# Kernel optimization log

Hardware: AMD Instinct MI355X
Metric: run time of the kernel (lower is better)

## Reference

```python
import jax, jax.numpy as jnp
import numpy as np

DIM = 768
HEADS = 12
HEAD_DIM = DIM // HEADS
HIDDEN = 4 * DIM
SCALE = HEAD_DIM ** -0.5
LN_EPS = 1e-5


def _fit_poly_gelu():
    # replicate PolyGELU.__init__: quadratic least-squares fit to exact GELU on [-3,3]
    x = np.linspace(-3.0, 3.0, 10000).astype(np.float32)
    y = np.asarray(jax.nn.gelu(jnp.asarray(x), approximate=False))
    X = np.stack([x ** 2, x, np.ones_like(x)], axis=1)
    c, *_ = np.linalg.lstsq(X, y, rcond=None)
    return c.astype(np.float32)  # [a, b, c]


def setup_inputs() -> dict:
    key = jax.random.key(0)
    ks = jax.random.split(key, 8)
    g = _fit_poly_gelu()
    w = lambda k, shp: (jax.random.normal(k, shp, dtype=jnp.float32) * 0.02)
    return {
        "x": jax.random.normal(ks[0], (4, 2048, DIM), dtype=jnp.float32),
        "ln1_g": jnp.ones((DIM,), jnp.float32),
        "ln1_b": jnp.zeros((DIM,), jnp.float32),
        "ln2_g": jnp.ones((DIM,), jnp.float32),
        "ln2_b": jnp.zeros((DIM,), jnp.float32),
        "qkv_w": w(ks[1], (DIM, 3 * DIM)),   # stored [in, out]
        "qkv_b": jnp.zeros((3 * DIM,), jnp.float32),
        "proj_w": w(ks[2], (DIM, DIM)),
        "proj_b": jnp.zeros((DIM,), jnp.float32),
        "fc1_w": w(ks[3], (DIM, HIDDEN)),
        "fc1_b": jnp.zeros((HIDDEN,), jnp.float32),
        "fc2_w": w(ks[4], (HIDDEN, DIM)),
        "fc2_b": jnp.zeros((DIM,), jnp.float32),
        "attn_a": jnp.float32(0.05),
        "attn_b": jnp.float32(0.5),
        "attn_c": jnp.float32(0.25),
        "gelu_a": jnp.float32(g[0]),
        "gelu_b": jnp.float32(g[1]),
        "gelu_c": jnp.float32(g[2]),
    }


def _layernorm(x, gamma, beta):
    mu = jnp.mean(x, axis=-1, keepdims=True)
    var = jnp.mean(jnp.square(x - mu), axis=-1, keepdims=True)
    return (x - mu) / jnp.sqrt(var + LN_EPS) * gamma + beta


def reference(x, ln1_g, ln1_b, ln2_g, ln2_b, qkv_w, qkv_b, proj_w, proj_b,
              fc1_w, fc1_b, fc2_w, fc2_b, attn_a, attn_b, attn_c,
              gelu_a, gelu_b, gelu_c):
    B, N, C = x.shape
    # --- attention branch ---
    h = _layernorm(x, ln1_g, ln1_b)
    qkv = (h @ qkv_w + qkv_b).reshape(B, N, 3, HEADS, HEAD_DIM)
    q, k, v = (qkv[:, :, i].transpose(0, 2, 1, 3) for i in range(3))  # [B,H,N,D]
    attn = jnp.einsum("bhnd,bhmd->bhnm", q, k) * SCALE
    # poly_normed: quadratic activation, clamp, row-normalize
    attn = attn_a * attn * attn + attn_b * attn + attn_c
    attn = jnp.maximum(attn, 1e-6)
    attn = attn / (jnp.sum(attn, axis=-1, keepdims=True) + 1e-8)
    out = jnp.einsum("bhnm,bhmd->bhnd", attn, v).transpose(0, 2, 1, 3).reshape(B, N, C)
    x = x + (out @ proj_w + proj_b)
    # --- MLP branch with PolyGELU ---
    h = _layernorm(x, ln2_g, ln2_b)
    u = h @ fc1_w + fc1_b
    u = gelu_a * u * u + gelu_b * u + gelu_c
    x = x + (u @ fc2_w + fc2_b)
    return x
```

## Files before the change

### kernel.cpp

```cpp
#include <hip/hip_runtime.h>

typedef __bf16 bf16x8 __attribute__((ext_vector_type(8)));
typedef __bf16 bf16x4 __attribute__((ext_vector_type(4)));
typedef float f32x4 __attribute__((ext_vector_type(4)));

#define LN_EPS 1e-5f

__device__ __forceinline__ void gl2lds16(const void* g, void* l) {
  __builtin_amdgcn_global_load_lds(
      (const __attribute__((address_space(1))) unsigned int*)g,
      (__attribute__((address_space(3))) unsigned int*)l, 16, 0, 0);
}

__global__ __launch_bounds__(256) void transpose_k(const float* __restrict__ in,
                                                   __bf16* __restrict__ out,
                                                   int R, int C) {
  __shared__ __bf16 t[32][33];
  int tx = threadIdx.x & 31, ty = threadIdx.x >> 5;
  int c = blockIdx.x * 32 + tx;
  for (int j = 0; j < 4; j++) {
    int r = blockIdx.y * 32 + ty + j * 8;
    t[ty + j * 8][tx] = (__bf16)in[(size_t)r * C + c];
  }
  __syncthreads();
  int r2 = blockIdx.y * 32 + tx;
  for (int j = 0; j < 4; j++) {
    int c2 = blockIdx.x * 32 + ty + j * 8;
    out[(size_t)c2 * R + r2] = t[tx][ty + j * 8];
  }
}

__global__ __launch_bounds__(256) void transpose_v(const __bf16* __restrict__ qkv,
                                                   __bf16* __restrict__ vt) {
  __shared__ __bf16 t[32][33];
  int bh = blockIdx.z;
  int b = bh / 12, h = bh % 12;
  int n0 = blockIdx.x * 32, d0 = blockIdx.y * 32;
  int tx = threadIdx.x & 31, ty = threadIdx.x >> 5;
  for (int j = 0; j < 4; j++) {
    int n = n0 + ty + j * 8;
    t[ty + j * 8][tx] = qkv[(size_t)(b * 2048 + n) * 2304 + 1536 + h * 64 + d0 + tx];
  }
  __syncthreads();
  for (int j = 0; j < 4; j++) {
    int d = d0 + ty + j * 8;
    vt[((size_t)bh * 64 + d) * 2048 + n0 + tx] = t[tx][ty + j * 8];
  }
}

__global__ __launch_bounds__(256) void ln_kernel(const float* __restrict__ x,
                                                 const float* __restrict__ g,
                                                 const float* __restrict__ bta,
                                                 __bf16* __restrict__ out) {
  int row = blockIdx.x;
  size_t base = (size_t)row * 768;
  int t = threadIdx.x;
  float v[3];
  float s = 0.f, s2 = 0.f;
  for (int k = 0; k < 3; k++) {
    float f = x[base + t + k * 256];
    v[k] = f;
    s += f;
    s2 += f * f;
  }
  for (int m = 1; m < 64; m <<= 1) {
    s += __shfl_xor(s, m, 64);
    s2 += __shfl_xor(s2, m, 64);
  }
  __shared__ float sm[4][2];
  int wid = t >> 6, lane = t & 63;
  if (lane == 0) { sm[wid][0] = s; sm[wid][1] = s2; }
  __syncthreads();
  s = sm[0][0] + sm[1][0] + sm[2][0] + sm[3][0];
  s2 = sm[0][1] + sm[1][1] + sm[2][1] + sm[3][1];
  float mu = s * (1.f / 768.f);
  float var = s2 * (1.f / 768.f) - mu * mu;
  float rstd = rsqrtf(var + LN_EPS);
  for (int k = 0; k < 3; k++) {
    int c = t + k * 256;
    out[base + c] = (__bf16)((v[k] - mu) * rstd * g[c] + bta[c]);
  }
}

template <int EPI>
__global__ __launch_bounds__(256) void gemm128(const __bf16* __restrict__ A,
                                               const __bf16* __restrict__ BT,
                                               const float* __restrict__ bias,
                                               const float* __restrict__ res,
                                               void* __restrict__ outv,
                                               int M, int N, int K,
                                               const float* __restrict__ c0p,
                                               const float* __restrict__ c1p,
                                               const float* __restrict__ c2p) {
  __shared__ __bf16 As[128][32];
  __shared__ __bf16 Bs[128][32];
  int tid = threadIdx.x;
  int lane = tid & 63, wid = tid >> 6;
  int wr = wid >> 1, wc = wid & 1;
  int m0 = blockIdx.y * 128, n0 = blockIdx.x * 128;
  int mr = lane & 15, kq = (lane >> 4) * 8;
  int srow = tid >> 2, scol = (tid & 3) * 8;

  f32x4 acc[4][4] = {};

  for (int k0 = 0; k0 < K; k0 += 32) {
    for (int i = 0; i < 2; i++) {
      int row = srow + i * 64;
      gl2lds16(&A[(size_t)(m0 + row) * K + k0 + scol], &As[row][scol]);
      gl2lds16(&BT[(size_t)(n0 + row) * K + k0 + scol], &Bs[row][scol]);
    }
    __syncthreads();
    bf16x8 af[4], bfr[4];
    for (int i = 0; i < 4; i++) af[i] = *(bf16x8*)&As[wr * 64 + i * 16 + mr][kq];
    for (int j = 0; j < 4; j++) bfr[j] = *(bf16x8*)&Bs[wc * 64 + j * 16 + mr][kq];
    for (int i = 0; i < 4; i++)
      for (int j = 0; j < 4; j++)
        acc[i][j] = __builtin_amdgcn_mfma_f32_16x16x32_bf16(af[i], bfr[j], acc[i][j], 0, 0, 0);
    __syncthreads();
  }

  float ga = 0.f, gb = 0.f, gc = 0.f;
  if (EPI == 1) { ga = *c0p; gb = *c1p; gc = *c2p; }

  for (int i = 0; i < 4; i++) {
    for (int j = 0; j < 4; j++) {
      int col = n0 + wc * 64 + j * 16 + mr;
      float bv = bias[col];
      for (int r = 0; r < 4; r++) {
        int row = m0 + wr * 64 + i * 16 + (lane >> 4) * 4 + r;
        size_t idx = (size_t)row * N + col;
        float c = acc[i][j][r] + bv;
        if (EPI == 0) {
          ((__bf16*)outv)[idx] = (__bf16)c;
        } else if (EPI == 1) {
          float u = (ga * c + gb) * c + gc;
          ((__bf16*)outv)[idx] = (__bf16)u;
        } else {
          ((float*)outv)[idx] = c + res[idx];
        }
      }
    }
  }
}

__global__ __launch_bounds__(256, 4) void attn_poly(const __bf16* __restrict__ qkv,
                                                    const __bf16* __restrict__ vt,
                                                    __bf16* __restrict__ outp,
                                                    const float* __restrict__ ap,
                                                    const float* __restrict__ bp,
                                                    const float* __restrict__ cp) {
  __shared__ __bf16 QPs[4][32][72];
  __shared__ __bf16 Ks[64][72];
  __shared__ __bf16 Vts[64][72];
  __bf16(*Qs)[72] = (__bf16(*)[72]) & QPs[0][0][0];

  int tid = threadIdx.x, lane = tid & 63, wid = tid >> 6;
  int mr = lane & 15, quad = lane >> 4, kq = quad * 8;
  int q0 = blockIdx.x * 128;
  int h = blockIdx.y, b = blockIdx.z;
  int bh = b * 12 + h;
  size_t baseQ = ((size_t)b * 2048) * 2304 + h * 64;

  for (int i = 0; i < 4; i++) {
    int chunk = tid + i * 256;
    int row = chunk >> 3, dc = chunk & 7;
    *(bf16x8*)&Qs[row][dc * 8] =
        *(const bf16x8*)&qkv[baseQ + (size_t)(q0 + row) * 2304 + dc * 8];
  }
  __syncthreads();

  bf16x8 qf[2][2];
  for (int i = 0; i < 2; i++)
    for (int s = 0; s < 2; s++)
      qf[i][s] = *(bf16x8*)&Qs[wid * 32 + i * 16 + mr][s * 32 + kq];

  float a2 = (*ap) * 0.015625f, b2 = (*bp) * 0.125f, cc = *cp;
  f32x4 o_acc[2][4] = {};
  float l_acc[2] = {0.f, 0.f};

  for (int kt = 0; kt < 32; kt++) {
    __syncthreads();
    for (int i = 0; i < 2; i++) {
      int chunk = tid + i * 256;
      int row = chunk >> 3, dc = chunk & 7;
      *(bf16x8*)&Ks[row][dc * 8] =
          *(const bf16x8*)&qkv[baseQ + (size_t)(kt * 64 + row) * 2304 + 768 + dc * 8];
      *(bf16x8*)&Vts[row][dc * 8] =
          *(const bf16x8*)&vt[((size_t)bh * 64 + row) * 2048 + kt * 64 + dc * 8];
    }
    __syncthreads();

    bf16x8 kf[4][2];
    for (int j = 0; j < 4; j++)
      for (int s = 0; s < 2; s++)
        kf[j][s] = *(bf16x8*)&Ks[j * 16 + mr][s * 32 + kq];

    for (int i = 0; i < 2; i++) {
      f32x4 sacc[4] = {};
      for (int j = 0; j < 4; j++)
        for (int s = 0; s < 2; s++)
          sacc[j] = __builtin_amdgcn_mfma_f32_16x16x32_bf16(kf[j][s], qf[i][s], sacc[j], 0, 0, 0);
      float rsum = 0.f;
      for (int j = 0; j < 4; j++) {
        bf16x4 pk;
        for (int r = 0; r < 4; r++) {
          float S = sacc[j][r];
          float p = fmaf(fmaf(a2, S, b2), S, cc);
          p = fmaxf(p, 1e-6f);
          rsum += p;
          pk[r] = (__bf16)p;
        }
        *(bf16x4*)&QPs[wid][i * 16 + mr][j * 16 + quad * 4] = pk;
      }
      rsum += __shfl_xor(rsum, 16, 64);
      rsum += __shfl_xor(rsum, 32, 64);
      l_acc[i] += rsum;
    }

    __syncthreads();

    for (int i = 0; i < 2; i++) {
      for (int s = 0; s < 2; s++) {
        bf16x8 pf = *(bf16x8*)&QPs[wid][i * 16 + mr][s * 32 + kq];
        for (int dt = 0; dt < 4; dt++) {
          bf16x8 vf = *(bf16x8*)&Vts[dt * 16 + mr][s * 32 + kq];
          o_acc[i][dt] = __builtin_amdgcn_mfma_f32_16x16x32_bf16(pf, vf, o_acc[i][dt], 0, 0, 0);
        }
      }
    }
  }

  size_t baseO = ((size_t)b * 2048) * 768 + h * 64;
  for (int i = 0; i < 2; i++) {
    float inv[4];
    for (int r = 0; r < 4; r++)
      inv[r] = 1.0f / (__shfl(l_acc[i], quad * 4 + r, 64) + 1e-8f);
    for (int dt = 0; dt < 4; dt++) {
      int q = q0 + wid * 32 + i * 16 + quad * 4;
      for (int r = 0; r < 4; r++) {
        outp[baseO + (size_t)(q + r) * 768 + dt * 16 + mr] =
            (__bf16)(o_acc[i][dt][r] * inv[r]);
      }
    }
  }
}

extern "C" void kernel_launch(void* const* d_in, const int* in_sizes, int n_in,
                              void* d_out, int out_size, void* d_ws, size_t ws_size,
                              hipStream_t stream) {
  const float* x     = (const float*)d_in[0];
  const float* ln1g  = (const float*)d_in[1];
  const float* ln1b  = (const float*)d_in[2];
  const float* ln2g  = (const float*)d_in[3];
  const float* ln2b  = (const float*)d_in[4];
  const float* qkvw  = (const float*)d_in[5];
  const float* qkvb  = (const float*)d_in[6];
  const float* projw = (const float*)d_in[7];
  const float* projb = (const float*)d_in[8];
  const float* fc1w  = (const float*)d_in[9];
  const float* fc1b  = (const float*)d_in[10];
  const float* fc2w  = (const float*)d_in[11];
  const float* fc2b  = (const float*)d_in[12];
  const float* attna = (const float*)d_in[13];
  const float* attnb = (const float*)d_in[14];
  const float* attnc = (const float*)d_in[15];
  const float* gelua = (const float*)d_in[16];
  const float* gelub = (const float*)d_in[17];
  const float* geluc = (const float*)d_in[18];

  char* ws = (char*)d_ws;
  __bf16* wT_qkv  = (__bf16*)(ws);
  __bf16* wT_proj = (__bf16*)(ws + 3538944);
  __bf16* wT_fc1  = (__bf16*)(ws + 4718592);
  __bf16* wT_fc2  = (__bf16*)(ws + 9437184);
  __bf16* h       = (__bf16*)(ws + 14155776);
  float*  x1      = (float*)(ws + 26738688);
  __bf16* qkvbuf  = (__bf16*)(ws + 51904512);
  __bf16* u       = (__bf16*)(ws + 51904512);
  __bf16* vtbuf   = (__bf16*)(ws + 89653248);
  float*  outp    = (float*)d_out;

  transpose_k<<<dim3(2304 / 32, 768 / 32), 256, 0, stream>>>(qkvw, wT_qkv, 768, 2304);
  transpose_k<<<dim3(768 / 32, 768 / 32), 256, 0, stream>>>(projw, wT_proj, 768, 768);
  transpose_k<<<dim3(3072 / 32, 768 / 32), 256, 0, stream>>>(fc1w, wT_fc1, 768, 3072);
  transpose_k<<<dim3(768 / 32, 3072 / 32), 256, 0, stream>>>(fc2w, wT_fc2, 3072, 768);

  ln_kernel<<<8192, 256, 0, stream>>>(x, ln1g, ln1b, h);
  gemm128<0><<<dim3(18, 64), 256, 0, stream>>>(h, wT_qkv, qkvb, nullptr, qkvbuf,
                                               8192, 2304, 768, nullptr, nullptr, nullptr);
  transpose_v<<<dim3(64, 2, 48), 256, 0, stream>>>(qkvbuf, vtbuf);
  attn_poly<<<dim3(16, 12, 4), 256, 0, stream>>>(qkvbuf, vtbuf, h, attna, attnb, attnc);
  gemm128<2><<<dim3(6, 64), 256, 0, stream>>>(h, wT_proj, projb, x, x1,
                                              8192, 768, 768, nullptr, nullptr, nullptr);
  ln_kernel<<<8192, 256, 0, stream>>>(x1, ln2g, ln2b, h);
  gemm128<1><<<dim3(24, 64), 256, 0, stream>>>(h, wT_fc1, fc1b, nullptr, u,
                                               8192, 3072, 768, gelua, gelub, geluc);
  gemm128<2><<<dim3(6, 64), 256, 0, stream>>>(u, wT_fc2, fc2b, x1, outp,
                                              8192, 768, 3072, nullptr, nullptr, nullptr);
}
```

Baseline: 480.3 us.

## Enlarge GEMM and attention tiles for QKV, FC1 and poly attention

Adds a gemm256 kernel with 128x256 output tiles, each wave holding a 4x8 MFMA accumulator grid, and uses it for the QKV and FC1 projections. The attention kernel now handles 256 queries per block (64 per wave) and keeps V fragments in registers across query sub-tiles, so each K/V tile loaded into LDS is reused by twice as many queries. The goal is less global and LDS traffic per MFMA. The cost is much higher register pressure (launch bounds lowered to 2 blocks), fewer blocks per grid, and possible spills.

```diff
diff --git a/kernel.cpp b/kernel.cpp
--- a/kernel.cpp
+++ b/kernel.cpp
@@ -143,25 +143,86 @@
   }
 }
 
-__global__ __launch_bounds__(256, 4) void attn_poly(const __bf16* __restrict__ qkv,
+template <int EPI>
+__global__ __launch_bounds__(256, 2) void gemm256(const __bf16* __restrict__ A,
+                                                  const __bf16* __restrict__ BT,
+                                                  const float* __restrict__ bias,
+                                                  void* __restrict__ outv,
+                                                  int M, int N, int K,
+                                                  const float* __restrict__ c0p,
+                                                  const float* __restrict__ c1p,
+                                                  const float* __restrict__ c2p) {
+  __shared__ __bf16 As[128][32];
+  __shared__ __bf16 Bs[256][32];
+  int tid = threadIdx.x;
+  int lane = tid & 63, wid = tid >> 6;
+  int wr = wid >> 1, wc = wid & 1;
+  int m0 = blockIdx.y * 128, n0 = blockIdx.x * 256;
+  int mr = lane & 15, quad = lane >> 4, kq = quad * 8;
+  int srow = tid >> 2, scol = (tid & 3) * 8;
+
+  f32x4 acc[4][8] = {};
+
+  for (int k0 = 0; k0 < K; k0 += 32) {
+    for (int i = 0; i < 2; i++) {
+      int row = srow + i * 64;
+      gl2lds16(&A[(size_t)(m0 + row) * K + k0 + scol], &As[row][scol]);
+    }
+    for (int i = 0; i < 4; i++) {
+      int row = srow + i * 64;
+      gl2lds16(&BT[(size_t)(n0 + row) * K + k0 + scol], &Bs[row][scol]);
+    }
+    __syncthreads();
+    bf16x8 af[4], bfr[8];
+    for (int i = 0; i < 4; i++) af[i] = *(bf16x8*)&As[wr * 64 + i * 16 + mr][kq];
+    for (int j = 0; j < 8; j++) bfr[j] = *(bf16x8*)&Bs[wc * 128 + j * 16 + mr][kq];
+    for (int i = 0; i < 4; i++)
+      for (int j = 0; j < 8; j++)
+        acc[i][j] = __builtin_amdgcn_mfma_f32_16x16x32_bf16(af[i], bfr[j], acc[i][j], 0, 0, 0);
+    __syncthreads();
+  }
+
+  float ga = 0.f, gb = 0.f, gc = 0.f;
+  if (EPI == 1) { ga = *c0p; gb = *c1p; gc = *c2p; }
+
+  for (int i = 0; i < 4; i++) {
+    for (int j = 0; j < 8; j++) {
+      int col = n0 + wc * 128 + j * 16 + mr;
+      float bv = bias[col];
+      for (int r = 0; r < 4; r++) {
+        int row = m0 + wr * 64 + i * 16 + quad * 4 + r;
+        size_t idx = (size_t)row * N + col;
+        float c = acc[i][j][r] + bv;
+        if (EPI == 0) {
+          ((__bf16*)outv)[idx] = (__bf16)c;
+        } else {
+          float u = (ga * c + gb) * c + gc;
+          ((__bf16*)outv)[idx] = (__bf16)u;
+        }
+      }
+    }
+  }
+}
+
+__global__ __launch_bounds__(256, 2) void attn_poly(const __bf16* __restrict__ qkv,
                                                     const __bf16* __restrict__ vt,
                                                     __bf16* __restrict__ outp,
                                                     const float* __restrict__ ap,
                                                     const float* __restrict__ bp,
                                                     const float* __restrict__ cp) {
-  __shared__ __bf16 QPs[4][32][72];
+  __shared__ __bf16 QPs[4][64][72];
   __shared__ __bf16 Ks[64][72];
   __shared__ __bf16 Vts[64][72];
   __bf16(*Qs)[72] = (__bf16(*)[72]) & QPs[0][0][0];
 
   int tid = threadIdx.x, lane = tid & 63, wid = tid >> 6;
   int mr = lane & 15, quad = lane >> 4, kq = quad * 8;
-  int q0 = blockIdx.x * 128;
+  int q0 = blockIdx.x * 256;
   int h = blockIdx.y, b = blockIdx.z;
   int bh = b * 12 + h;
   size_t baseQ = ((size_t)b * 2048) * 2304 + h * 64;
 
-  for (int i = 0; i < 4; i++) {
+  for (int i = 0; i < 8; i++) {
     int chunk = tid + i * 256;
     int row = chunk >> 3, dc = chunk & 7;
     *(bf16x8*)&Qs[row][dc * 8] =
@@ -169,14 +230,14 @@
   }
   __syncthreads();
 
-  bf16x8 qf[2][2];
-  for (int i = 0; i < 2; i++)
+  bf16x8 qf[4][2];
+  for (int i = 0; i < 4; i++)
     for (int s = 0; s < 2; s++)
-      qf[i][s] = *(bf16x8*)&Qs[wid * 32 + i * 16 + mr][s * 32 + kq];
+      qf[i][s] = *(bf16x8*)&Qs[wid * 64 + i * 16 + mr][s * 32 + kq];
 
   float a2 = (*ap) * 0.015625f, b2 = (*bp) * 0.125f, cc = *cp;
-  f32x4 o_acc[2][4] = {};
-  float l_acc[2] = {0.f, 0.f};
+  f32x4 o_acc[4][4] = {};
+  float l_acc[4] = {0.f, 0.f, 0.f, 0.f};
 
   for (int kt = 0; kt < 32; kt++) {
     __syncthreads();
@@ -194,8 +255,12 @@
     for (int j = 0; j < 4; j++)
       for (int s = 0; s < 2; s++)
         kf[j][s] = *(bf16x8*)&Ks[j * 16 + mr][s * 32 + kq];
-
-    for (int i = 0; i < 2; i++) {
+    bf16x8 vf[2][4];
+    for (int s = 0; s < 2; s++)
+      for (int dt = 0; dt < 4; dt++)
+        vf[s][dt] = *(bf16x8*)&Vts[dt * 16 + mr][s * 32 + kq];
+
+    for (int i = 0; i < 4; i++) {
       f32x4 sacc[4] = {};
       for (int j = 0; j < 4; j++)
         for (int s = 0; s < 2; s++)
@@ -219,24 +284,22 @@
 
     __syncthreads();
 
-    for (int i = 0; i < 2; i++) {
+    for (int i = 0; i < 4; i++) {
       for (int s = 0; s < 2; s++) {
         bf16x8 pf = *(bf16x8*)&QPs[wid][i * 16 + mr][s * 32 + kq];
-        for (int dt = 0; dt < 4; dt++) {
-          bf16x8 vf = *(bf16x8*)&Vts[dt * 16 + mr][s * 32 + kq];
-          o_acc[i][dt] = __builtin_amdgcn_mfma_f32_16x16x32_bf16(pf, vf, o_acc[i][dt], 0, 0, 0);
-        }
+        for (int dt = 0; dt < 4; dt++)
+          o_acc[i][dt] = __builtin_amdgcn_mfma_f32_16x16x32_bf16(pf, vf[s][dt], o_acc[i][dt], 0, 0, 0);
       }
     }
   }
 
   size_t baseO = ((size_t)b * 2048) * 768 + h * 64;
-  for (int i = 0; i < 2; i++) {
+  for (int i = 0; i < 4; i++) {
     float inv[4];
     for (int r = 0; r < 4; r++)
       inv[r] = 1.0f / (__shfl(l_acc[i], quad * 4 + r, 64) + 1e-8f);
     for (int dt = 0; dt < 4; dt++) {
-      int q = q0 + wid * 32 + i * 16 + quad * 4;
+      int q = q0 + wid * 64 + i * 16 + quad * 4;
       for (int r = 0; r < 4; r++) {
         outp[baseO + (size_t)(q + r) * 768 + dt * 16 + mr] =
             (__bf16)(o_acc[i][dt][r] * inv[r]);
@@ -286,14 +349,14 @@
   transpose_k<<<dim3(768 / 32, 3072 / 32), 256, 0, stream>>>(fc2w, wT_fc2, 3072, 768);
 
   ln_kernel<<<8192, 256, 0, stream>>>(x, ln1g, ln1b, h);
-  gemm128<0><<<dim3(18, 64), 256, 0, stream>>>(h, wT_qkv, qkvb, nullptr, qkvbuf,
-                                               8192, 2304, 768, nullptr, nullptr, nullptr);
+  gemm256<0><<<dim3(9, 64), 256, 0, stream>>>(h, wT_qkv, qkvb, qkvbuf,
+                                              8192, 2304, 768, nullptr, nullptr, nullptr);
   transpose_v<<<dim3(64, 2, 48), 256, 0, stream>>>(qkvbuf, vtbuf);
-  attn_poly<<<dim3(16, 12, 4), 256, 0, stream>>>(qkvbuf, vtbuf, h, attna, attnb, attnc);
+  attn_poly<<<dim3(8, 12, 4), 256, 0, stream>>>(qkvbuf, vtbuf, h, attna, attnb, attnc);
   gemm128<2><<<dim3(6, 64), 256, 0, stream>>>(h, wT_proj, projb, x, x1,
                                               8192, 768, 768, nullptr, nullptr, nullptr);
   ln_kernel<<<8192, 256, 0, stream>>>(x1, ln2g, ln2b, h);
-  gemm128<1><<<dim3(24, 64), 256, 0, stream>>>(h, wT_fc1, fc1b, nullptr, u,
+  gemm256<1><<<dim3(12, 64), 256, 0, stream>>>(h, wT_fc1, fc1b, u,
                                                8192, 3072, 768, gelua, gelub, geluc);
   gemm128<2><<<dim3(6, 64), 256, 0, stream>>>(u, wT_fc2, fc2b, x1, outp,
                                               8192, 768, 3072, nullptr, nullptr, nullptr);
```

Measured after the change: 480.7 us. No clear change (+0.1%).
